# Kernel optimization log

Measured on AMD Instinct MI355X. Metric: run time of the kernel, lower is better.

The kernel has to match this reference:

```python
import jax, jax.numpy as jnp
import numpy as np

N_NODES, E, M_CELLS = 100000, 400000, 50000
D_IN, D_H, D_OUT = 384, 256, 256


def setup_inputs() -> dict:
    key = jax.random.key(0)
    ks = jax.random.split(key, 13)
    s = 0.02
    return {
        "chunk_features": jax.random.normal(ks[0], (N_NODES, D_IN), jnp.float32),
        "flat_nodes_t": jax.random.randint(ks[1], (E,), 0, N_NODES),
        "cell_asgn_t": jax.random.randint(ks[2], (E,), 0, M_CELLS),
        "M": M_CELLS,
        # phi: Linear(D_IN,D_H)+ReLU, Linear(D_H,D_H)+ReLU
        "W1": jax.random.normal(ks[3], (D_IN, D_H), jnp.float32) * s,
        "b1": jnp.zeros((D_H,), jnp.float32),
        "W2": jax.random.normal(ks[4], (D_H, D_H), jnp.float32) * s,
        "b2": jnp.zeros((D_H,), jnp.float32),
        # rho: Linear(D_H,D_H)+ReLU, Linear(D_H,D_H)+ReLU, Linear(D_H,D_OUT)
        "R1": jax.random.normal(ks[5], (D_H, D_H), jnp.float32) * s,
        "c1": jnp.zeros((D_H,), jnp.float32),
        "R2": jax.random.normal(ks[6], (D_H, D_H), jnp.float32) * s,
        "c2": jnp.zeros((D_H,), jnp.float32),
        "R3": jax.random.normal(ks[7], (D_H, D_OUT), jnp.float32) * s,
        "c3": jnp.zeros((D_OUT,), jnp.float32),
    }


def reference(chunk_features, flat_nodes_t, cell_asgn_t, M,
              W1, b1, W2, b2, R1, c1, R2, c2, R3, c3):
    # gather node features per cell-membership: [E, D_IN]
    x = chunk_features[flat_nodes_t]
    # phi MLP
    h = jax.nn.relu(x @ W1 + b1)
    h = jax.nn.relu(h @ W2 + b2)            # [E, D_H]
    # scatter-add per cell (torch scatter_add_ into zeros)
    cell_sums = jax.ops.segment_sum(h, cell_asgn_t, num_segments=M)  # [M, D_H]
    # rho MLP
    r = jax.nn.relu(cell_sums @ R1 + c1)
    r = jax.nn.relu(r @ R2 + c2)
    return r @ R3 + c3                      # [M, D_OUT]
```

## Files before the change

kernel.cpp:

```cpp
#include <hip/hip_runtime.h>

typedef unsigned short u16;
typedef __bf16 bf16x8 __attribute__((ext_vector_type(8)));
typedef float f32x4 __attribute__((ext_vector_type(4)));

__device__ __forceinline__ u16 f2bf(float f) {
  unsigned int u = __builtin_bit_cast(unsigned int, f);
  u += 0x7fffu + ((u >> 16) & 1u);
  return (u16)(u >> 16);
}
__device__ __forceinline__ float bf2f(u16 h) {
  unsigned int u = ((unsigned int)h) << 16;
  return __builtin_bit_cast(float, u);
}

__global__ __launch_bounds__(256) void k_prep(
    const float* __restrict__ W1, const float* __restrict__ W2,
    const float* __restrict__ R1, const float* __restrict__ R2, const float* __restrict__ R3,
    u16* __restrict__ W1s, u16* __restrict__ W2s,
    u16* __restrict__ R1s, u16* __restrict__ R2s, u16* __restrict__ R3s) {
  int t = blockIdx.x * 256 + threadIdx.x;
  const float* src; u16* dst; int lt;
  if (t < 12288) { src = W1; dst = W1s; lt = t; }
  else {
    int u = t - 12288;
    int m = u >> 13;
    lt = u & 8191;
    if (m == 0)      { src = W2; dst = W2s; }
    else if (m == 1) { src = R1; dst = R1s; }
    else if (m == 2) { src = R2; dst = R2s; }
    else if (m == 3) { src = R3; dst = R3s; }
    else return;
  }
  int lane = lt & 63;
  int nt = (lt >> 6) & 15;
  int ks = lt >> 10;
  int col = nt * 16 + (lane & 15);
  int kb = ks * 32 + (lane >> 4) * 8;
  union { u16 u[8]; uint4 v; } o;
#pragma unroll
  for (int j = 0; j < 8; ++j) o.u[j] = f2bf(src[(size_t)(kb + j) * 256 + col]);
  *(uint4*)(dst + (size_t)lt * 8) = o.v;
}

__global__ __launch_bounds__(256) void k_hist(const int* __restrict__ cells,
                                              int* __restrict__ counts, int E) {
  int e = blockIdx.x * 256 + threadIdx.x;
  if (e < E) atomicAdd(&counts[cells[e]], 1);
}

__global__ __launch_bounds__(256) void k_scan1(const int* __restrict__ counts,
                                               int* __restrict__ offs,
                                               int* __restrict__ bsum, int M) {
  __shared__ int ws[4];
  int tid = threadIdx.x, lane = tid & 63, wid = tid >> 6;
  int i = blockIdx.x * 256 + tid;
  int v = (i < M) ? counts[i] : 0;
  int x = v;
#pragma unroll
  for (int s = 1; s < 64; s <<= 1) { int y = __shfl_up(x, s); if (lane >= s) x += y; }
  if (lane == 63) ws[wid] = x;
  __syncthreads();
  int pre = 0;
#pragma unroll
  for (int w = 0; w < 4; ++w) if (w < wid) pre += ws[w];
  if (i < M) offs[i] = pre + x - v;
  if (tid == 255) bsum[blockIdx.x] = pre + x;
}

__global__ __launch_bounds__(256) void k_scan2(int* __restrict__ bsum, int nb) {
  __shared__ int ws[4];
  int tid = threadIdx.x, lane = tid & 63, wid = tid >> 6;
  int v = (tid < nb) ? bsum[tid] : 0;
  int x = v;
#pragma unroll
  for (int s = 1; s < 64; s <<= 1) { int y = __shfl_up(x, s); if (lane >= s) x += y; }
  if (lane == 63) ws[wid] = x;
  __syncthreads();
  int pre = 0;
#pragma unroll
  for (int w = 0; w < 4; ++w) if (w < wid) pre += ws[w];
  if (tid < nb) bsum[tid] = pre + x - v;
}

__global__ __launch_bounds__(256) void k_scan3(int* __restrict__ offs,
                                               const int* __restrict__ bsum,
                                               int* __restrict__ cursor, int M, int E) {
  int i = blockIdx.x * 256 + threadIdx.x;
  if (i < M) { int o = offs[i] + bsum[blockIdx.x]; offs[i] = o; cursor[i] = o; }
  if (i == M) offs[M] = E;
}

__global__ __launch_bounds__(256) void k_scatter(const int* __restrict__ cells,
                                                 const int* __restrict__ nodes,
                                                 int* __restrict__ cursor,
                                                 int* __restrict__ sorted, int E) {
  int e = blockIdx.x * 256 + threadIdx.x;
  if (e < E) {
    int c = cells[e];
    int p = atomicAdd(&cursor[c], 1);
    sorted[p] = nodes[e];
  }
}

__global__ __launch_bounds__(256) void k_phi(
    const float* __restrict__ X,
    const u16* __restrict__ W1s, const float* __restrict__ b1,
    const u16* __restrict__ W2s, const float* __restrict__ b2,
    u16* __restrict__ H, int N) {
  __shared__ __align__(16) u16 buf[64 * 256];
  const int tid = threadIdx.x, lane = tid & 63, wid = tid >> 6;
  const int g = lane >> 4, r16 = lane & 15;
  const int rbase = blockIdx.x * 64;
  const int swz = r16 << 3;

  const u16* w1p = W1s + (size_t)(wid * 4) * 512 + lane * 8;
  const u16* w2p = W2s + (size_t)(wid * 4) * 512 + lane * 8;

  {
    f32x4 xr[16];
#pragma unroll
    for (int it = 0; it < 16; ++it) {
      int u = it * 256 + tid;
      int row = u >> 6, c4 = u & 63;
      int crow = rbase + row; crow = crow < N ? crow : N - 1;
      xr[it] = *(const f32x4*)(X + (size_t)crow * 384 + c4 * 4);
    }
#pragma unroll
    for (int it = 0; it < 16; ++it) {
      int u = it * 256 + tid;
      int row = u >> 6, c4 = u & 63;
      uint2 pk;
      pk.x = (unsigned int)f2bf(xr[it][0]) | ((unsigned int)f2bf(xr[it][1]) << 16);
      pk.y = (unsigned int)f2bf(xr[it][2]) | ((unsigned int)f2bf(xr[it][3]) << 16);
      *(uint2*)(buf + row * 256 + ((c4 * 4) ^ ((row & 15) << 3))) = pk;
    }
  }
  __syncthreads();

  f32x4 acc[4][4];
#pragma unroll
  for (int m = 0; m < 4; ++m)
#pragma unroll
    for (int n = 0; n < 4; ++n) acc[m][n] = (f32x4){0.f, 0.f, 0.f, 0.f};

#pragma unroll 1
  for (int ks = 0; ks < 8; ++ks) {
    bf16x8 bfr[4];
#pragma unroll
    for (int n = 0; n < 4; ++n)
      bfr[n] = *(const bf16x8*)(w1p + (size_t)ks * 8192 + n * 512);
    const u16* bp = buf + ((ks * 32 + g * 8) ^ swz);
#pragma unroll
    for (int m = 0; m < 4; ++m) {
      bf16x8 af = *(const bf16x8*)(bp + (m * 16 + r16) * 256);
#pragma unroll
      for (int n = 0; n < 4; ++n)
        acc[m][n] = __builtin_amdgcn_mfma_f32_16x16x32_bf16(af, bfr[n], acc[m][n], 0, 0, 0);
    }
  }
  __syncthreads();

  {
    f32x4 xr[8];
#pragma unroll
    for (int it = 0; it < 8; ++it) {
      int u = it * 256 + tid;
      int row = u >> 5, c4 = u & 31;
      int crow = rbase + row; crow = crow < N ? crow : N - 1;
      xr[it] = *(const f32x4*)(X + (size_t)crow * 384 + 256 + c4 * 4);
    }
#pragma unroll
    for (int it = 0; it < 8; ++it) {
      int u = it * 256 + tid;
      int row = u >> 5, c4 = u & 31;
      uint2 pk;
      pk.x = (unsigned int)f2bf(xr[it][0]) | ((unsigned int)f2bf(xr[it][1]) << 16);
      pk.y = (unsigned int)f2bf(xr[it][2]) | ((unsigned int)f2bf(xr[it][3]) << 16);
      *(uint2*)(buf + row * 256 + ((c4 * 4) ^ ((row & 15) << 3))) = pk;
    }
  }
  __syncthreads();

#pragma unroll 1
  for (int ksl = 0; ksl < 4; ++ksl) {
    bf16x8 bfr[4];
#pragma unroll
    for (int n = 0; n < 4; ++n)
      bfr[n] = *(const bf16x8*)(w1p + (size_t)(8 + ksl) * 8192 + n * 512);
    const u16* bp = buf + ((ksl * 32 + g * 8) ^ swz);
#pragma unroll
    for (int m = 0; m < 4; ++m) {
      bf16x8 af = *(const bf16x8*)(bp + (m * 16 + r16) * 256);
#pragma unroll
      for (int n = 0; n < 4; ++n)
        acc[m][n] = __builtin_amdgcn_mfma_f32_16x16x32_bf16(af, bfr[n], acc[m][n], 0, 0, 0);
    }
  }
  __syncthreads();

  float bias1[4];
#pragma unroll
  for (int n = 0; n < 4; ++n) bias1[n] = b1[wid * 64 + n * 16 + r16];
#pragma unroll
  for (int m = 0; m < 4; ++m)
#pragma unroll
    for (int n = 0; n < 4; ++n)
#pragma unroll
      for (int rr = 0; rr < 4; ++rr) {
        int row = m * 16 + g * 4 + rr;
        int col = wid * 64 + n * 16 + r16;
        float v = fmaxf(acc[m][n][rr] + bias1[n], 0.f);
        buf[row * 256 + (col ^ ((row & 15) << 3))] = f2bf(v);
      }
  __syncthreads();

#pragma unroll
  for (int m = 0; m < 4; ++m)
#pragma unroll
    for (int n = 0; n < 4; ++n) acc[m][n] = (f32x4){0.f, 0.f, 0.f, 0.f};
#pragma unroll 1
  for (int ks = 0; ks < 8; ++ks) {
    bf16x8 bfr[4];
#pragma unroll
    for (int n = 0; n < 4; ++n)
      bfr[n] = *(const bf16x8*)(w2p + (size_t)ks * 8192 + n * 512);
    const u16* bp = buf + ((ks * 32 + g * 8) ^ swz);
#pragma unroll
    for (int m = 0; m < 4; ++m) {
      bf16x8 af = *(const bf16x8*)(bp + (m * 16 + r16) * 256);
#pragma unroll
      for (int n = 0; n < 4; ++n)
        acc[m][n] = __builtin_amdgcn_mfma_f32_16x16x32_bf16(af, bfr[n], acc[m][n], 0, 0, 0);
    }
  }
  __syncthreads();

  float bias2[4];
#pragma unroll
  for (int n = 0; n < 4; ++n) bias2[n] = b2[wid * 64 + n * 16 + r16];
#pragma unroll
  for (int m = 0; m < 4; ++m)
#pragma unroll
    for (int n = 0; n < 4; ++n)
#pragma unroll
      for (int rr = 0; rr < 4; ++rr) {
        int row = m * 16 + g * 4 + rr;
        int col = wid * 64 + n * 16 + r16;
        float v = fmaxf(acc[m][n][rr] + bias2[n], 0.f);
        buf[row * 256 + (col ^ ((row & 15) << 3))] = f2bf(v);
      }
  __syncthreads();

#pragma unroll 4
  for (int it = 0; it < 8; ++it) {
    int u = it * 256 + tid;
    int row = u >> 5, k8 = u & 31;
    uint4 d = *(const uint4*)(buf + row * 256 + ((k8 * 8) ^ ((row & 15) << 3)));
    int grow = rbase + row;
    if (grow < N) *(uint4*)(H + (size_t)grow * 256 + k8 * 8) = d;
  }
}

__global__ __launch_bounds__(256) void k_cellsum(
    const u16* __restrict__ H, const int* __restrict__ sorted,
    const int* __restrict__ offs, u16* __restrict__ CS, int M) {
  const int lane = threadIdx.x & 63, wid = threadIdx.x >> 6;
  int c = blockIdx.x * 4 + wid;
  if (c >= M) return;
  int s = offs[c], e = offs[c + 1];
  float a0 = 0.f, a1 = 0.f, a2 = 0.f, a3 = 0.f;
  for (int base = s; base < e; base += 64) {
    int cnt = e - base; if (cnt > 64) cnt = 64;
    int idx = sorted[base + (lane < cnt ? lane : 0)];
    int j = 0;
    for (; j + 8 <= cnt; j += 8) {
      ushort4 h[8];
#pragma unroll
      for (int q = 0; q < 8; ++q) {
        int nd = __shfl(idx, j + q);
        h[q] = *(const ushort4*)(H + (size_t)nd * 256 + lane * 4);
      }
#pragma unroll
      for (int q = 0; q < 8; ++q) {
        a0 += bf2f(h[q].x); a1 += bf2f(h[q].y);
        a2 += bf2f(h[q].z); a3 += bf2f(h[q].w);
      }
    }
    if (j + 4 <= cnt) {
      ushort4 h[4];
#pragma unroll
      for (int q = 0; q < 4; ++q) {
        int nd = __shfl(idx, j + q);
        h[q] = *(const ushort4*)(H + (size_t)nd * 256 + lane * 4);
      }
#pragma unroll
      for (int q = 0; q < 4; ++q) {
        a0 += bf2f(h[q].x); a1 += bf2f(h[q].y);
        a2 += bf2f(h[q].z); a3 += bf2f(h[q].w);
      }
      j += 4;
    }
    for (; j < cnt; ++j) {
      int nd = __shfl(idx, j);
      ushort4 h = *(const ushort4*)(H + (size_t)nd * 256 + lane * 4);
      a0 += bf2f(h.x); a1 += bf2f(h.y); a2 += bf2f(h.z); a3 += bf2f(h.w);
    }
  }
  ushort4 o;
  o.x = f2bf(a0); o.y = f2bf(a1); o.z = f2bf(a2); o.w = f2bf(a3);
  *(ushort4*)(CS + (size_t)c * 256 + lane * 4) = o;
}

__global__ __launch_bounds__(256) void k_rho(
    const u16* __restrict__ CS,
    const u16* __restrict__ R1s, const float* __restrict__ c1,
    const u16* __restrict__ R2s, const float* __restrict__ c2,
    const u16* __restrict__ R3s, const float* __restrict__ c3,
    float* __restrict__ OUT, int M) {
  __shared__ __align__(16) u16 buf[64 * 256];
  const int tid = threadIdx.x, lane = tid & 63, wid = tid >> 6;
  const int g = lane >> 4, r16 = lane & 15;
  const int rbase = blockIdx.x * 64;
  const int swz = r16 << 3;

  const u16* w1p = R1s + (size_t)(wid * 4) * 512 + lane * 8;
  const u16* w2p = R2s + (size_t)(wid * 4) * 512 + lane * 8;
  const u16* w3p = R3s + (size_t)(wid * 4) * 512 + lane * 8;

  {
    uint4 xr[8];
#pragma unroll
    for (int it = 0; it < 8; ++it) {
      int u = it * 256 + tid;
      int row = u >> 5, k8 = u & 31;
      int crow = rbase + row; crow = crow < M ? crow : M - 1;
      xr[it] = *(const uint4*)(CS + (size_t)crow * 256 + k8 * 8);
    }
#pragma unroll
    for (int it = 0; it < 8; ++it) {
      int u = it * 256 + tid;
      int row = u >> 5, k8 = u & 31;
      *(uint4*)(buf + row * 256 + ((k8 * 8) ^ ((row & 15) << 3))) = xr[it];
    }
  }
  __syncthreads();

  f32x4 acc[4][4];

#pragma unroll
  for (int m = 0; m < 4; ++m)
#pragma unroll
    for (int n = 0; n < 4; ++n) acc[m][n] = (f32x4){0.f, 0.f, 0.f, 0.f};
#pragma unroll 1
  for (int ks = 0; ks < 8; ++ks) {
    bf16x8 bfr[4];
#pragma unroll
    for (int n = 0; n < 4; ++n)
      bfr[n] = *(const bf16x8*)(w1p + (size_t)ks * 8192 + n * 512);
    const u16* bp = buf + ((ks * 32 + g * 8) ^ swz);
#pragma unroll
    for (int m = 0; m < 4; ++m) {
      bf16x8 af = *(const bf16x8*)(bp + (m * 16 + r16) * 256);
#pragma unroll
      for (int n = 0; n < 4; ++n)
        acc[m][n] = __builtin_amdgcn_mfma_f32_16x16x32_bf16(af, bfr[n], acc[m][n], 0, 0, 0);
    }
  }
  __syncthreads();

  float bias1[4];
#pragma unroll
  for (int n = 0; n < 4; ++n) bias1[n] = c1[wid * 64 + n * 16 + r16];
#pragma unroll
  for (int m = 0; m < 4; ++m)
#pragma unroll
    for (int n = 0; n < 4; ++n)
#pragma unroll
      for (int rr = 0; rr < 4; ++rr) {
        int row = m * 16 + g * 4 + rr;
        int col = wid * 64 + n * 16 + r16;
        float v = fmaxf(acc[m][n][rr] + bias1[n], 0.f);
        buf[row * 256 + (col ^ ((row & 15) << 3))] = f2bf(v);
      }
  __syncthreads();

#pragma unroll
  for (int m = 0; m < 4; ++m)
#pragma unroll
    for (int n = 0; n < 4; ++n) acc[m][n] = (f32x4){0.f, 0.f, 0.f, 0.f};
#pragma unroll 1
  for (int ks = 0; ks < 8; ++ks) {
    bf16x8 bfr[4];
#pragma unroll
    for (int n = 0; n < 4; ++n)
      bfr[n] = *(const bf16x8*)(w2p + (size_t)ks * 8192 + n * 512);
    const u16* bp = buf + ((ks * 32 + g * 8) ^ swz);
#pragma unroll
    for (int m = 0; m < 4; ++m) {
      bf16x8 af = *(const bf16x8*)(bp + (m * 16 + r16) * 256);
#pragma unroll
      for (int n = 0; n < 4; ++n)
        acc[m][n] = __builtin_amdgcn_mfma_f32_16x16x32_bf16(af, bfr[n], acc[m][n], 0, 0, 0);
    }
  }
  __syncthreads();

  float bias2[4];
#pragma unroll
  for (int n = 0; n < 4; ++n) bias2[n] = c2[wid * 64 + n * 16 + r16];
#pragma unroll
  for (int m = 0; m < 4; ++m)
#pragma unroll
    for (int n = 0; n < 4; ++n)
#pragma unroll
      for (int rr = 0; rr < 4; ++rr) {
        int row = m * 16 + g * 4 + rr;
        int col = wid * 64 + n * 16 + r16;
        float v = fmaxf(acc[m][n][rr] + bias2[n], 0.f);
        buf[row * 256 + (col ^ ((row & 15) << 3))] = f2bf(v);
      }
  __syncthreads();

#pragma unroll
  for (int m = 0; m < 4; ++m)
#pragma unroll
    for (int n = 0; n < 4; ++n) acc[m][n] = (f32x4){0.f, 0.f, 0.f, 0.f};
#pragma unroll 1
  for (int ks = 0; ks < 8; ++ks) {
    bf16x8 bfr[4];
#pragma unroll
    for (int n = 0; n < 4; ++n)
      bfr[n] = *(const bf16x8*)(w3p + (size_t)ks * 8192 + n * 512);
    const u16* bp = buf + ((ks * 32 + g * 8) ^ swz);
#pragma unroll
    for (int m = 0; m < 4; ++m) {
      bf16x8 af = *(const bf16x8*)(bp + (m * 16 + r16) * 256);
#pragma unroll
      for (int n = 0; n < 4; ++n)
        acc[m][n] = __builtin_amdgcn_mfma_f32_16x16x32_bf16(af, bfr[n], acc[m][n], 0, 0, 0);
    }
  }
#pragma unroll
  for (int n = 0; n < 4; ++n) {
    float bias = c3[wid * 64 + n * 16 + r16];
#pragma unroll
    for (int m = 0; m < 4; ++m)
#pragma unroll
      for (int rr = 0; rr < 4; ++rr) {
        int grow = rbase + m * 16 + g * 4 + rr;
        if (grow < M) OUT[(size_t)grow * 256 + wid * 64 + n * 16 + r16] = acc[m][n][rr] + bias;
      }
  }
}

extern "C" void kernel_launch(void* const* d_in, const int* in_sizes, int n_in,
                              void* d_out, int out_size, void* d_ws, size_t ws_size,
                              hipStream_t stream) {
  const float* X    = (const float*)d_in[0];
  const int* nodes  = (const int*)d_in[1];
  const int* cells  = (const int*)d_in[2];
  const float* W1   = (const float*)d_in[4];
  const float* b1   = (const float*)d_in[5];
  const float* W2   = (const float*)d_in[6];
  const float* b2   = (const float*)d_in[7];
  const float* R1   = (const float*)d_in[8];
  const float* c1   = (const float*)d_in[9];
  const float* R2   = (const float*)d_in[10];
  const float* c2   = (const float*)d_in[11];
  const float* R3   = (const float*)d_in[12];
  const float* c3   = (const float*)d_in[13];
  float* OUT = (float*)d_out;

  const int N = in_sizes[0] / 384;
  const int E = in_sizes[1];
  const int M = out_size / 256;

  char* ws = (char*)d_ws;
  size_t off = 0;
  auto alloc = [&](size_t b) { size_t o = off; off += (b + 255) & ~(size_t)255; return o; };
  u16* W1s    = (u16*)(ws + alloc((size_t)12 * 16 * 64 * 8 * 2));
  u16* W2s    = (u16*)(ws + alloc((size_t)8 * 16 * 64 * 8 * 2));
  u16* R1s    = (u16*)(ws + alloc((size_t)8 * 16 * 64 * 8 * 2));
  u16* R2s    = (u16*)(ws + alloc((size_t)8 * 16 * 64 * 8 * 2));
  u16* R3s    = (u16*)(ws + alloc((size_t)8 * 16 * 64 * 8 * 2));
  u16* H      = (u16*)(ws + alloc((size_t)N * 256 * 2));
  u16* CS     = (u16*)(ws + alloc((size_t)M * 256 * 2));
  int* counts = (int*)(ws + alloc((size_t)M * 4));
  int* offs   = (int*)(ws + alloc((size_t)(M + 1) * 4));
  int* cursor = (int*)(ws + alloc((size_t)M * 4));
  int* sorted = (int*)(ws + alloc((size_t)E * 4));
  int* bsum   = (int*)(ws + alloc((size_t)256 * 4));

  const int NB = (M + 255) / 256;

  hipMemsetAsync(counts, 0, (size_t)M * 4, stream);
  k_prep<<<176, 256, 0, stream>>>(W1, W2, R1, R2, R3, W1s, W2s, R1s, R2s, R3s);
  k_hist<<<(E + 255) / 256, 256, 0, stream>>>(cells, counts, E);
  k_scan1<<<NB, 256, 0, stream>>>(counts, offs, bsum, M);
  k_scan2<<<1, 256, 0, stream>>>(bsum, NB);
  k_scan3<<<(M + 256) / 256, 256, 0, stream>>>(offs, bsum, cursor, M, E);
  k_scatter<<<(E + 255) / 256, 256, 0, stream>>>(cells, nodes, cursor, sorted, E);
  k_phi<<<(N + 63) / 64, 256, 0, stream>>>(X, W1s, b1, W2s, b2, H, N);
  k_cellsum<<<(M + 3) / 4, 256, 0, stream>>>(H, sorted, offs, CS, M);
  k_rho<<<(M + 63) / 64, 256, 0, stream>>>(CS, R1s, c1, R2s, c2, R3s, c3, OUT, M);
}
```

Baseline: 222.0 us.

## Make phi and rho MLP kernels persistent with register-prefetched next tiles

Converts the phi and rho MLP kernels into persistent grid-stride loops over 32-row tiles, prefetching the next tile's inputs into registers while the current tile's GEMMs run, with separate LDS buffers for input and hidden activations. Biases are hoisted out of the loop, and the phi kernel stages the full 384-wide input at once instead of in two halves. The goal is to hide global-load latency behind MFMA work and cut per-block launch and prologue cost. In exchange each block uses smaller tiles with less weight reuse per tile, and the fixed grid sizes (1024 and 512 blocks) may not balance evenly across CUs.

```diff
diff --git a/kernel.cpp b/kernel.cpp
--- a/kernel.cpp
+++ b/kernel.cpp
@@ -108,157 +108,137 @@
     const u16* __restrict__ W1s, const float* __restrict__ b1,
     const u16* __restrict__ W2s, const float* __restrict__ b2,
     u16* __restrict__ H, int N) {
-  __shared__ __align__(16) u16 buf[64 * 256];
+  __shared__ __align__(16) u16 xbuf[32 * 384];
+  __shared__ __align__(16) u16 hbuf[32 * 256];
   const int tid = threadIdx.x, lane = tid & 63, wid = tid >> 6;
   const int g = lane >> 4, r16 = lane & 15;
-  const int rbase = blockIdx.x * 64;
   const int swz = r16 << 3;
+  const int T = (N + 31) >> 5;
+  const int step = gridDim.x;
 
   const u16* w1p = W1s + (size_t)(wid * 4) * 512 + lane * 8;
   const u16* w2p = W2s + (size_t)(wid * 4) * 512 + lane * 8;
 
-  {
-    f32x4 xr[16];
-#pragma unroll
-    for (int it = 0; it < 16; ++it) {
+  float bias1[4], bias2[4];
+#pragma unroll
+  for (int n = 0; n < 4; ++n) {
+    bias1[n] = b1[wid * 64 + n * 16 + r16];
+    bias2[n] = b2[wid * 64 + n * 16 + r16];
+  }
+
+  f32x4 xr[12];
+
+  auto issue = [&](int t) {
+#pragma unroll
+    for (int it = 0; it < 12; ++it) {
       int u = it * 256 + tid;
-      int row = u >> 6, c4 = u & 63;
-      int crow = rbase + row; crow = crow < N ? crow : N - 1;
+      int row = u / 96, c4 = u - row * 96;
+      int crow = t * 32 + row; crow = crow < N ? crow : N - 1;
       xr[it] = *(const f32x4*)(X + (size_t)crow * 384 + c4 * 4);
     }
-#pragma unroll
-    for (int it = 0; it < 16; ++it) {
+  };
+  auto stagewrite = [&]() {
+#pragma unroll
+    for (int it = 0; it < 12; ++it) {
       int u = it * 256 + tid;
-      int row = u >> 6, c4 = u & 63;
+      int row = u / 96, c4 = u - row * 96;
       uint2 pk;
       pk.x = (unsigned int)f2bf(xr[it][0]) | ((unsigned int)f2bf(xr[it][1]) << 16);
       pk.y = (unsigned int)f2bf(xr[it][2]) | ((unsigned int)f2bf(xr[it][3]) << 16);
-      *(uint2*)(buf + row * 256 + ((c4 * 4) ^ ((row & 15) << 3))) = pk;
-    }
-  }
+      *(uint2*)(xbuf + row * 384 + ((c4 * 4) ^ ((row & 15) << 3))) = pk;
+    }
+  };
+
+  const int t0 = blockIdx.x;
+  if (t0 >= T) return;
+
+  issue(t0);
+  stagewrite();
   __syncthreads();
-
-  f32x4 acc[4][4];
-#pragma unroll
-  for (int m = 0; m < 4; ++m)
-#pragma unroll
-    for (int n = 0; n < 4; ++n) acc[m][n] = (f32x4){0.f, 0.f, 0.f, 0.f};
-
-#pragma unroll 1
-  for (int ks = 0; ks < 8; ++ks) {
-    bf16x8 bfr[4];
-#pragma unroll
-    for (int n = 0; n < 4; ++n)
-      bfr[n] = *(const bf16x8*)(w1p + (size_t)ks * 8192 + n * 512);
-    const u16* bp = buf + ((ks * 32 + g * 8) ^ swz);
-#pragma unroll
-    for (int m = 0; m < 4; ++m) {
-      bf16x8 af = *(const bf16x8*)(bp + (m * 16 + r16) * 256);
-#pragma unroll
-      for (int n = 0; n < 4; ++n)
-        acc[m][n] = __builtin_amdgcn_mfma_f32_16x16x32_bf16(af, bfr[n], acc[m][n], 0, 0, 0);
-    }
-  }
-  __syncthreads();
-
-  {
-    f32x4 xr[8];
-#pragma unroll
-    for (int it = 0; it < 8; ++it) {
+  issue(t0 + step);
+
+  for (int t = t0; t < T; t += step) {
+    f32x4 acc[2][4];
+#pragma unroll
+    for (int m = 0; m < 2; ++m)
+#pragma unroll
+      for (int n = 0; n < 4; ++n) acc[m][n] = (f32x4){0.f, 0.f, 0.f, 0.f};
+#pragma unroll 4
+    for (int ks = 0; ks < 12; ++ks) {
+      bf16x8 bfr[4];
+#pragma unroll
+      for (int n = 0; n < 4; ++n)
+        bfr[n] = *(const bf16x8*)(w1p + (size_t)ks * 8192 + n * 512);
+      const u16* bp = xbuf + ((ks * 32 + g * 8) ^ swz);
+#pragma unroll
+      for (int m = 0; m < 2; ++m) {
+        bf16x8 af = *(const bf16x8*)(bp + (m * 16 + r16) * 384);
+#pragma unroll
+        for (int n = 0; n < 4; ++n)
+          acc[m][n] = __builtin_amdgcn_mfma_f32_16x16x32_bf16(af, bfr[n], acc[m][n], 0, 0, 0);
+      }
+    }
+    __syncthreads();
+
+    stagewrite();
+
+#pragma unroll
+    for (int m = 0; m < 2; ++m)
+#pragma unroll
+      for (int n = 0; n < 4; ++n)
+#pragma unroll
+        for (int rr = 0; rr < 4; ++rr) {
+          int row = m * 16 + g * 4 + rr;
+          int col = wid * 64 + n * 16 + r16;
+          float v = fmaxf(acc[m][n][rr] + bias1[n], 0.f);
+          hbuf[row * 256 + (col ^ ((row & 15) << 3))] = f2bf(v);
+        }
+    __syncthreads();
+
+    issue(t + 2 * step);
+
+#pragma unroll
+    for (int m = 0; m < 2; ++m)
+#pragma unroll
+      for (int n = 0; n < 4; ++n) acc[m][n] = (f32x4){0.f, 0.f, 0.f, 0.f};
+#pragma unroll 4
+    for (int ks = 0; ks < 8; ++ks) {
+      bf16x8 bfr[4];
+#pragma unroll
+      for (int n = 0; n < 4; ++n)
+        bfr[n] = *(const bf16x8*)(w2p + (size_t)ks * 8192 + n * 512);
+      const u16* bp = hbuf + ((ks * 32 + g * 8) ^ swz);
+#pragma unroll
+      for (int m = 0; m < 2; ++m) {
+        bf16x8 af = *(const bf16x8*)(bp + (m * 16 + r16) * 256);
+#pragma unroll
+        for (int n = 0; n < 4; ++n)
+          acc[m][n] = __builtin_amdgcn_mfma_f32_16x16x32_bf16(af, bfr[n], acc[m][n], 0, 0, 0);
+      }
+    }
+    __syncthreads();
+
+#pragma unroll
+    for (int m = 0; m < 2; ++m)
+#pragma unroll
+      for (int n = 0; n < 4; ++n)
+#pragma unroll
+        for (int rr = 0; rr < 4; ++rr) {
+          int row = m * 16 + g * 4 + rr;
+          int col = wid * 64 + n * 16 + r16;
+          float v = fmaxf(acc[m][n][rr] + bias2[n], 0.f);
+          hbuf[row * 256 + (col ^ ((row & 15) << 3))] = f2bf(v);
+        }
+    __syncthreads();
+
+#pragma unroll
+    for (int it = 0; it < 4; ++it) {
       int u = it * 256 + tid;
-      int row = u >> 5, c4 = u & 31;
-      int crow = rbase + row; crow = crow < N ? crow : N - 1;
-      xr[it] = *(const f32x4*)(X + (size_t)crow * 384 + 256 + c4 * 4);
-    }
-#pragma unroll
-    for (int it = 0; it < 8; ++it) {
-      int u = it * 256 + tid;
-      int row = u >> 5, c4 = u & 31;
-      uint2 pk;
-      pk.x = (unsigned int)f2bf(xr[it][0]) | ((unsigned int)f2bf(xr[it][1]) << 16);
-      pk.y = (unsigned int)f2bf(xr[it][2]) | ((unsigned int)f2bf(xr[it][3]) << 16);
-      *(uint2*)(buf + row * 256 + ((c4 * 4) ^ ((row & 15) << 3))) = pk;
-    }
-  }
-  __syncthreads();
-
-#pragma unroll 1
-  for (int ksl = 0; ksl < 4; ++ksl) {
-    bf16x8 bfr[4];
-#pragma unroll
-    for (int n = 0; n < 4; ++n)
-      bfr[n] = *(const bf16x8*)(w1p + (size_t)(8 + ksl) * 8192 + n * 512);
-    const u16* bp = buf + ((ksl * 32 + g * 8) ^ swz);
-#pragma unroll
-    for (int m = 0; m < 4; ++m) {
-      bf16x8 af = *(const bf16x8*)(bp + (m * 16 + r16) * 256);
-#pragma unroll
-      for (int n = 0; n < 4; ++n)
-        acc[m][n] = __builtin_amdgcn_mfma_f32_16x16x32_bf16(af, bfr[n], acc[m][n], 0, 0, 0);
-    }
-  }
-  __syncthreads();
-
-  float bias1[4];
-#pragma unroll
-  for (int n = 0; n < 4; ++n) bias1[n] = b1[wid * 64 + n * 16 + r16];
-#pragma unroll
-  for (int m = 0; m < 4; ++m)
-#pragma unroll
-    for (int n = 0; n < 4; ++n)
-#pragma unroll
-      for (int rr = 0; rr < 4; ++rr) {
-        int row = m * 16 + g * 4 + rr;
-        int col = wid * 64 + n * 16 + r16;
-        float v = fmaxf(acc[m][n][rr] + bias1[n], 0.f);
-        buf[row * 256 + (col ^ ((row & 15) << 3))] = f2bf(v);
-      }
-  __syncthreads();
-
-#pragma unroll
-  for (int m = 0; m < 4; ++m)
-#pragma unroll
-    for (int n = 0; n < 4; ++n) acc[m][n] = (f32x4){0.f, 0.f, 0.f, 0.f};
-#pragma unroll 1
-  for (int ks = 0; ks < 8; ++ks) {
-    bf16x8 bfr[4];
-#pragma unroll
-    for (int n = 0; n < 4; ++n)
-      bfr[n] = *(const bf16x8*)(w2p + (size_t)ks * 8192 + n * 512);
-    const u16* bp = buf + ((ks * 32 + g * 8) ^ swz);
-#pragma unroll
-    for (int m = 0; m < 4; ++m) {
-      bf16x8 af = *(const bf16x8*)(bp + (m * 16 + r16) * 256);
-#pragma unroll
-      for (int n = 0; n < 4; ++n)
-        acc[m][n] = __builtin_amdgcn_mfma_f32_16x16x32_bf16(af, bfr[n], acc[m][n], 0, 0, 0);
-    }
-  }
-  __syncthreads();
-
-  float bias2[4];
-#pragma unroll
-  for (int n = 0; n < 4; ++n) bias2[n] = b2[wid * 64 + n * 16 + r16];
-#pragma unroll
-  for (int m = 0; m < 4; ++m)
-#pragma unroll
-    for (int n = 0; n < 4; ++n)
-#pragma unroll
-      for (int rr = 0; rr < 4; ++rr) {
-        int row = m * 16 + g * 4 + rr;
-        int col = wid * 64 + n * 16 + r16;
-        float v = fmaxf(acc[m][n][rr] + bias2[n], 0.f);
-        buf[row * 256 + (col ^ ((row & 15) << 3))] = f2bf(v);
-      }
-  __syncthreads();
-
-#pragma unroll 4
-  for (int it = 0; it < 8; ++it) {
-    int u = it * 256 + tid;
-    int row = u >> 5, k8 = u & 31;
-    uint4 d = *(const uint4*)(buf + row * 256 + ((k8 * 8) ^ ((row & 15) << 3)));
-    int grow = rbase + row;
-    if (grow < N) *(uint4*)(H + (size_t)grow * 256 + k8 * 8) = d;
+      int row = u >> 5, k8 = u & 31;
+      uint4 d = *(const uint4*)(hbuf + row * 256 + ((k8 * 8) ^ ((row & 15) << 3)));
+      int grow = t * 32 + row;
+      if (grow < N) *(uint4*)(H + (size_t)grow * 256 + k8 * 8) = d;
+    }
   }
 }
 
@@ -318,139 +298,157 @@
     const u16* __restrict__ R2s, const float* __restrict__ c2,
     const u16* __restrict__ R3s, const float* __restrict__ c3,
     float* __restrict__ OUT, int M) {
-  __shared__ __align__(16) u16 buf[64 * 256];
+  __shared__ __align__(16) u16 xbuf[32 * 256];
+  __shared__ __align__(16) u16 hbuf[32 * 256];
   const int tid = threadIdx.x, lane = tid & 63, wid = tid >> 6;
   const int g = lane >> 4, r16 = lane & 15;
-  const int rbase = blockIdx.x * 64;
   const int swz = r16 << 3;
+  const int T = (M + 31) >> 5;
+  const int step = gridDim.x;
 
   const u16* w1p = R1s + (size_t)(wid * 4) * 512 + lane * 8;
   const u16* w2p = R2s + (size_t)(wid * 4) * 512 + lane * 8;
   const u16* w3p = R3s + (size_t)(wid * 4) * 512 + lane * 8;
 
-  {
-    uint4 xr[8];
-#pragma unroll
-    for (int it = 0; it < 8; ++it) {
+  float bias1[4], bias2[4], bias3[4];
+#pragma unroll
+  for (int n = 0; n < 4; ++n) {
+    bias1[n] = c1[wid * 64 + n * 16 + r16];
+    bias2[n] = c2[wid * 64 + n * 16 + r16];
+    bias3[n] = c3[wid * 64 + n * 16 + r16];
+  }
+
+  uint4 xr[4];
+  auto issue = [&](int t) {
+#pragma unroll
+    for (int it = 0; it < 4; ++it) {
       int u = it * 256 + tid;
       int row = u >> 5, k8 = u & 31;
-      int crow = rbase + row; crow = crow < M ? crow : M - 1;
+      int crow = t * 32 + row; crow = crow < M ? crow : M - 1;
       xr[it] = *(const uint4*)(CS + (size_t)crow * 256 + k8 * 8);
     }
-#pragma unroll
-    for (int it = 0; it < 8; ++it) {
+  };
+  auto stagewrite = [&]() {
+#pragma unroll
+    for (int it = 0; it < 4; ++it) {
       int u = it * 256 + tid;
       int row = u >> 5, k8 = u & 31;
-      *(uint4*)(buf + row * 256 + ((k8 * 8) ^ ((row & 15) << 3))) = xr[it];
-    }
-  }
+      *(uint4*)(xbuf + row * 256 + ((k8 * 8) ^ ((row & 15) << 3))) = xr[it];
+    }
+  };
+
+  const int t0 = blockIdx.x;
+  if (t0 >= T) return;
+  issue(t0);
+  stagewrite();
   __syncthreads();
-
-  f32x4 acc[4][4];
-
-#pragma unroll
-  for (int m = 0; m < 4; ++m)
-#pragma unroll
-    for (int n = 0; n < 4; ++n) acc[m][n] = (f32x4){0.f, 0.f, 0.f, 0.f};
-#pragma unroll 1
-  for (int ks = 0; ks < 8; ++ks) {
-    bf16x8 bfr[4];
-#pragma unroll
-    for (int n = 0; n < 4; ++n)
-      bfr[n] = *(const bf16x8*)(w1p + (size_t)ks * 8192 + n * 512);
-    const u16* bp = buf + ((ks * 32 + g * 8) ^ swz);
-#pragma unroll
-    for (int m = 0; m < 4; ++m) {
-      bf16x8 af = *(const bf16x8*)(bp + (m * 16 + r16) * 256);
-#pragma unroll
-      for (int n = 0; n < 4; ++n)
-        acc[m][n] = __builtin_amdgcn_mfma_f32_16x16x32_bf16(af, bfr[n], acc[m][n], 0, 0, 0);
-    }
-  }
-  __syncthreads();
-
-  float bias1[4];
-#pragma unroll
-  for (int n = 0; n < 4; ++n) bias1[n] = c1[wid * 64 + n * 16 + r16];
-#pragma unroll
-  for (int m = 0; m < 4; ++m)
-#pragma unroll
-    for (int n = 0; n < 4; ++n)
-#pragma unroll
-      for (int rr = 0; rr < 4; ++rr) {
-        int row = m * 16 + g * 4 + rr;
-        int col = wid * 64 + n * 16 + r16;
-        float v = fmaxf(acc[m][n][rr] + bias1[n], 0.f);
-        buf[row * 256 + (col ^ ((row & 15) << 3))] = f2bf(v);
-      }
-  __syncthreads();
-
-#pragma unroll
-  for (int m = 0; m < 4; ++m)
-#pragma unroll
-    for (int n = 0; n < 4; ++n) acc[m][n] = (f32x4){0.f, 0.f, 0.f, 0.f};
-#pragma unroll 1
-  for (int ks = 0; ks < 8; ++ks) {
-    bf16x8 bfr[4];
-#pragma unroll
-    for (int n = 0; n < 4; ++n)
-      bfr[n] = *(const bf16x8*)(w2p + (size_t)ks * 8192 + n * 512);
-    const u16* bp = buf + ((ks * 32 + g * 8) ^ swz);
-#pragma unroll
-    for (int m = 0; m < 4; ++m) {
-      bf16x8 af = *(const bf16x8*)(bp + (m * 16 + r16) * 256);
-#pragma unroll
-      for (int n = 0; n < 4; ++n)
-        acc[m][n] = __builtin_amdgcn_mfma_f32_16x16x32_bf16(af, bfr[n], acc[m][n], 0, 0, 0);
-    }
-  }
-  __syncthreads();
-
-  float bias2[4];
-#pragma unroll
-  for (int n = 0; n < 4; ++n) bias2[n] = c2[wid * 64 + n * 16 + r16];
-#pragma unroll
-  for (int m = 0; m < 4; ++m)
-#pragma unroll
-    for (int n = 0; n < 4; ++n)
-#pragma unroll
-      for (int rr = 0; rr < 4; ++rr) {
-        int row = m * 16 + g * 4 + rr;
-        int col = wid * 64 + n * 16 + r16;
-        float v = fmaxf(acc[m][n][rr] + bias2[n], 0.f);
-        buf[row * 256 + (col ^ ((row & 15) << 3))] = f2bf(v);
-      }
-  __syncthreads();
-
-#pragma unroll
-  for (int m = 0; m < 4; ++m)
-#pragma unroll
-    for (int n = 0; n < 4; ++n) acc[m][n] = (f32x4){0.f, 0.f, 0.f, 0.f};
-#pragma unroll 1
-  for (int ks = 0; ks < 8; ++ks) {
-    bf16x8 bfr[4];
-#pragma unroll
-    for (int n = 0; n < 4; ++n)
-      bfr[n] = *(const bf16x8*)(w3p + (size_t)ks * 8192 + n * 512);
-    const u16* bp = buf + ((ks * 32 + g * 8) ^ swz);
-#pragma unroll
-    for (int m = 0; m < 4; ++m) {
-      bf16x8 af = *(const bf16x8*)(bp + (m * 16 + r16) * 256);
-#pragma unroll
-      for (int n = 0; n < 4; ++n)
-        acc[m][n] = __builtin_amdgcn_mfma_f32_16x16x32_bf16(af, bfr[n], acc[m][n], 0, 0, 0);
-    }
-  }
-#pragma unroll
-  for (int n = 0; n < 4; ++n) {
-    float bias = c3[wid * 64 + n * 16 + r16];
-#pragma unroll
-    for (int m = 0; m < 4; ++m)
-#pragma unroll
-      for (int rr = 0; rr < 4; ++rr) {
-        int grow = rbase + m * 16 + g * 4 + rr;
-        if (grow < M) OUT[(size_t)grow * 256 + wid * 64 + n * 16 + r16] = acc[m][n][rr] + bias;
-      }
+  issue(t0 + step);
+
+  for (int t = t0; t < T; t += step) {
+    f32x4 acc[2][4];
+
+#pragma unroll
+    for (int m = 0; m < 2; ++m)
+#pragma unroll
+      for (int n = 0; n < 4; ++n) acc[m][n] = (f32x4){0.f, 0.f, 0.f, 0.f};
+#pragma unroll 4
+    for (int ks = 0; ks < 8; ++ks) {
+      bf16x8 bfr[4];
+#pragma unroll
+      for (int n = 0; n < 4; ++n)
+        bfr[n] = *(const bf16x8*)(w1p + (size_t)ks * 8192 + n * 512);
+      const u16* bp = xbuf + ((ks * 32 + g * 8) ^ swz);
+#pragma unroll
+      for (int m = 0; m < 2; ++m) {
+        bf16x8 af = *(const bf16x8*)(bp + (m * 16 + r16) * 256);
+#pragma unroll
+        for (int n = 0; n < 4; ++n)
+          acc[m][n] = __builtin_amdgcn_mfma_f32_16x16x32_bf16(af, bfr[n], acc[m][n], 0, 0, 0);
+      }
+    }
+    __syncthreads();
+
+    stagewrite();
+
+#pragma unroll
+    for (int m = 0; m < 2; ++m)
+#pragma unroll
+      for (int n = 0; n < 4; ++n)
+#pragma unroll
+        for (int rr = 0; rr < 4; ++rr) {
+          int row = m * 16 + g * 4 + rr;
+          int col = wid * 64 + n * 16 + r16;
+          float v = fmaxf(acc[m][n][rr] + bias1[n], 0.f);
+          hbuf[row * 256 + (col ^ ((row & 15) << 3))] = f2bf(v);
+        }
+    __syncthreads();
+
+    issue(t + 2 * step);
+
+#pragma unroll
+    for (int m = 0; m < 2; ++m)
+#pragma unroll
+      for (int n = 0; n < 4; ++n) acc[m][n] = (f32x4){0.f, 0.f, 0.f, 0.f};
+#pragma unroll 4
+    for (int ks = 0; ks < 8; ++ks) {
+      bf16x8 bfr[4];
+#pragma unroll
+      for (int n = 0; n < 4; ++n)
+        bfr[n] = *(const bf16x8*)(w2p + (size_t)ks * 8192 + n * 512);
+      const u16* bp = hbuf + ((ks * 32 + g * 8) ^ swz);
+#pragma unroll
+      for (int m = 0; m < 2; ++m) {
+        bf16x8 af = *(const bf16x8*)(bp + (m * 16 + r16) * 256);
+#pragma unroll
+        for (int n = 0; n < 4; ++n)
+          acc[m][n] = __builtin_amdgcn_mfma_f32_16x16x32_bf16(af, bfr[n], acc[m][n], 0, 0, 0);
+      }
+    }
+    __syncthreads();
+
+#pragma unroll
+    for (int m = 0; m < 2; ++m)
+#pragma unroll
+      for (int n = 0; n < 4; ++n)
+#pragma unroll
+        for (int rr = 0; rr < 4; ++rr) {
+          int row = m * 16 + g * 4 + rr;
+          int col = wid * 64 + n * 16 + r16;
+          float v = fmaxf(acc[m][n][rr] + bias2[n], 0.f);
+          hbuf[row * 256 + (col ^ ((row & 15) << 3))] = f2bf(v);
+        }
+    __syncthreads();
+
+#pragma unroll
+    for (int m = 0; m < 2; ++m)
+#pragma unroll
+      for (int n = 0; n < 4; ++n) acc[m][n] = (f32x4){0.f, 0.f, 0.f, 0.f};
+#pragma unroll 4
+    for (int ks = 0; ks < 8; ++ks) {
+      bf16x8 bfr[4];
+#pragma unroll
+      for (int n = 0; n < 4; ++n)
+        bfr[n] = *(const bf16x8*)(w3p + (size_t)ks * 8192 + n * 512);
+      const u16* bp = hbuf + ((ks * 32 + g * 8) ^ swz);
+#pragma unroll
+      for (int m = 0; m < 2; ++m) {
+        bf16x8 af = *(const bf16x8*)(bp + (m * 16 + r16) * 256);
+#pragma unroll
+        for (int n = 0; n < 4; ++n)
+          acc[m][n] = __builtin_amdgcn_mfma_f32_16x16x32_bf16(af, bfr[n], acc[m][n], 0, 0, 0);
+      }
+    }
+#pragma unroll
+    for (int n = 0; n < 4; ++n) {
+#pragma unroll
+      for (int m = 0; m < 2; ++m)
+#pragma unroll
+        for (int rr = 0; rr < 4; ++rr) {
+          int grow = t * 32 + m * 16 + g * 4 + rr;
+          if (grow < M)
+            OUT[(size_t)grow * 256 + wid * 64 + n * 16 + r16] = acc[m][n][rr] + bias3[n];
+        }
+    }
   }
 }
 
@@ -501,7 +499,7 @@
   k_scan2<<<1, 256, 0, stream>>>(bsum, NB);
   k_scan3<<<(M + 256) / 256, 256, 0, stream>>>(offs, bsum, cursor, M, E);
   k_scatter<<<(E + 255) / 256, 256, 0, stream>>>(cells, nodes, cursor, sorted, E);
-  k_phi<<<(N + 63) / 64, 256, 0, stream>>>(X, W1s, b1, W2s, b2, H, N);
+  k_phi<<<1024, 256, 0, stream>>>(X, W1s, b1, W2s, b2, H, N);
   k_cellsum<<<(M + 3) / 4, 256, 0, stream>>>(H, sorted, offs, CS, M);
-  k_rho<<<(M + 63) / 64, 256, 0, stream>>>(CS, R1s, c1, R2s, c2, R3s, c3, OUT, M);
-}
+  k_rho<<<512, 256, 0, stream>>>(CS, R1s, c1, R2s, c2, R3s, c3, OUT, M);
+}
```

After: 219.0 us. About the same (-1.3%).

## Use 1024-thread blocks with 128-row tiles in phi and rho MLP kernels

Applied to the files above, without the earlier changes.

Both fused MLP kernels now process 128 rows per block with 16 waves instead of 64 rows with 4 waves. Each wave owns one 16-column slice across all 128 rows, so it loads one weight fragment per k-step and reuses it across 8 row tiles. The aim is to halve weight traffic per row and amortise the activation staging over more rows. The cost is a larger LDS buffer (64KB), fewer accumulators and fewer weight fragments per wave, and possibly lower occupancy with 1024-thread blocks.

```diff
diff --git a/kernel.cpp b/kernel.cpp
--- a/kernel.cpp
+++ b/kernel.cpp
@@ -103,32 +103,35 @@
   }
 }
 
-__global__ __launch_bounds__(256) void k_phi(
+__global__ __launch_bounds__(1024) void k_phi_big(
     const float* __restrict__ X,
     const u16* __restrict__ W1s, const float* __restrict__ b1,
     const u16* __restrict__ W2s, const float* __restrict__ b2,
     u16* __restrict__ H, int N) {
-  __shared__ __align__(16) u16 buf[64 * 256];
+  __shared__ __align__(16) u16 buf[128 * 256];
   const int tid = threadIdx.x, lane = tid & 63, wid = tid >> 6;
   const int g = lane >> 4, r16 = lane & 15;
-  const int rbase = blockIdx.x * 64;
   const int swz = r16 << 3;
-
-  const u16* w1p = W1s + (size_t)(wid * 4) * 512 + lane * 8;
-  const u16* w2p = W2s + (size_t)(wid * 4) * 512 + lane * 8;
+  const int rbase = blockIdx.x * 128;
+
+  const u16* w1p = W1s + (size_t)wid * 512 + lane * 8;
+  const u16* w2p = W2s + (size_t)wid * 512 + lane * 8;
+
+  const float bias1 = b1[wid * 16 + r16];
+  const float bias2 = b2[wid * 16 + r16];
 
   {
-    f32x4 xr[16];
-#pragma unroll
-    for (int it = 0; it < 16; ++it) {
-      int u = it * 256 + tid;
+    f32x4 xr[8];
+#pragma unroll
+    for (int it = 0; it < 8; ++it) {
+      int u = it * 1024 + tid;
       int row = u >> 6, c4 = u & 63;
       int crow = rbase + row; crow = crow < N ? crow : N - 1;
       xr[it] = *(const f32x4*)(X + (size_t)crow * 384 + c4 * 4);
     }
 #pragma unroll
-    for (int it = 0; it < 16; ++it) {
-      int u = it * 256 + tid;
+    for (int it = 0; it < 8; ++it) {
+      int u = it * 1024 + tid;
       int row = u >> 6, c4 = u & 63;
       uint2 pk;
       pk.x = (unsigned int)f2bf(xr[it][0]) | ((unsigned int)f2bf(xr[it][1]) << 16);
@@ -138,41 +141,34 @@
   }
   __syncthreads();
 
-  f32x4 acc[4][4];
-#pragma unroll
-  for (int m = 0; m < 4; ++m)
-#pragma unroll
-    for (int n = 0; n < 4; ++n) acc[m][n] = (f32x4){0.f, 0.f, 0.f, 0.f};
-
-#pragma unroll 1
+  f32x4 acc[8];
+#pragma unroll
+  for (int m = 0; m < 8; ++m) acc[m] = (f32x4){0.f, 0.f, 0.f, 0.f};
+
+#pragma unroll 2
   for (int ks = 0; ks < 8; ++ks) {
-    bf16x8 bfr[4];
-#pragma unroll
-    for (int n = 0; n < 4; ++n)
-      bfr[n] = *(const bf16x8*)(w1p + (size_t)ks * 8192 + n * 512);
+    bf16x8 bfr = *(const bf16x8*)(w1p + (size_t)ks * 8192);
     const u16* bp = buf + ((ks * 32 + g * 8) ^ swz);
 #pragma unroll
-    for (int m = 0; m < 4; ++m) {
-      bf16x8 af = *(const bf16x8*)(bp + (m * 16 + r16) * 256);
-#pragma unroll
-      for (int n = 0; n < 4; ++n)
-        acc[m][n] = __builtin_amdgcn_mfma_f32_16x16x32_bf16(af, bfr[n], acc[m][n], 0, 0, 0);
+    for (int m = 0; m < 8; ++m) {
+      bf16x8 af = *(const bf16x8*)(bp + (m * 16 + r16) * 256);
+      acc[m] = __builtin_amdgcn_mfma_f32_16x16x32_bf16(af, bfr, acc[m], 0, 0, 0);
     }
   }
   __syncthreads();
 
   {
-    f32x4 xr[8];
-#pragma unroll
-    for (int it = 0; it < 8; ++it) {
-      int u = it * 256 + tid;
+    f32x4 xr[4];
+#pragma unroll
+    for (int it = 0; it < 4; ++it) {
+      int u = it * 1024 + tid;
       int row = u >> 5, c4 = u & 31;
       int crow = rbase + row; crow = crow < N ? crow : N - 1;
       xr[it] = *(const f32x4*)(X + (size_t)crow * 384 + 256 + c4 * 4);
     }
 #pragma unroll
-    for (int it = 0; it < 8; ++it) {
-      int u = it * 256 + tid;
+    for (int it = 0; it < 4; ++it) {
+      int u = it * 1024 + tid;
       int row = u >> 5, c4 = u & 31;
       uint2 pk;
       pk.x = (unsigned int)f2bf(xr[it][0]) | ((unsigned int)f2bf(xr[it][1]) << 16);
@@ -182,79 +178,57 @@
   }
   __syncthreads();
 
-#pragma unroll 1
+#pragma unroll
   for (int ksl = 0; ksl < 4; ++ksl) {
-    bf16x8 bfr[4];
-#pragma unroll
-    for (int n = 0; n < 4; ++n)
-      bfr[n] = *(const bf16x8*)(w1p + (size_t)(8 + ksl) * 8192 + n * 512);
+    bf16x8 bfr = *(const bf16x8*)(w1p + (size_t)(8 + ksl) * 8192);
     const u16* bp = buf + ((ksl * 32 + g * 8) ^ swz);
 #pragma unroll
-    for (int m = 0; m < 4; ++m) {
-      bf16x8 af = *(const bf16x8*)(bp + (m * 16 + r16) * 256);
-#pragma unroll
-      for (int n = 0; n < 4; ++n)
-        acc[m][n] = __builtin_amdgcn_mfma_f32_16x16x32_bf16(af, bfr[n], acc[m][n], 0, 0, 0);
-    }
-  }
-  __syncthreads();
-
-  float bias1[4];
-#pragma unroll
-  for (int n = 0; n < 4; ++n) bias1[n] = b1[wid * 64 + n * 16 + r16];
-#pragma unroll
-  for (int m = 0; m < 4; ++m)
-#pragma unroll
-    for (int n = 0; n < 4; ++n)
-#pragma unroll
-      for (int rr = 0; rr < 4; ++rr) {
-        int row = m * 16 + g * 4 + rr;
-        int col = wid * 64 + n * 16 + r16;
-        float v = fmaxf(acc[m][n][rr] + bias1[n], 0.f);
-        buf[row * 256 + (col ^ ((row & 15) << 3))] = f2bf(v);
-      }
-  __syncthreads();
-
-#pragma unroll
-  for (int m = 0; m < 4; ++m)
-#pragma unroll
-    for (int n = 0; n < 4; ++n) acc[m][n] = (f32x4){0.f, 0.f, 0.f, 0.f};
-#pragma unroll 1
+    for (int m = 0; m < 8; ++m) {
+      bf16x8 af = *(const bf16x8*)(bp + (m * 16 + r16) * 256);
+      acc[m] = __builtin_amdgcn_mfma_f32_16x16x32_bf16(af, bfr, acc[m], 0, 0, 0);
+    }
+  }
+  __syncthreads();
+
+#pragma unroll
+  for (int m = 0; m < 8; ++m)
+#pragma unroll
+    for (int rr = 0; rr < 4; ++rr) {
+      int row = m * 16 + g * 4 + rr;
+      int col = wid * 16 + r16;
+      float v = fmaxf(acc[m][rr] + bias1, 0.f);
+      buf[row * 256 + (col ^ ((row & 15) << 3))] = f2bf(v);
+    }
+  __syncthreads();
+
+#pragma unroll
+  for (int m = 0; m < 8; ++m) acc[m] = (f32x4){0.f, 0.f, 0.f, 0.f};
+#pragma unroll 2
   for (int ks = 0; ks < 8; ++ks) {
-    bf16x8 bfr[4];
-#pragma unroll
-    for (int n = 0; n < 4; ++n)
-      bfr[n] = *(const bf16x8*)(w2p + (size_t)ks * 8192 + n * 512);
+    bf16x8 bfr = *(const bf16x8*)(w2p + (size_t)ks * 8192);
     const u16* bp = buf + ((ks * 32 + g * 8) ^ swz);
 #pragma unroll
-    for (int m = 0; m < 4; ++m) {
-      bf16x8 af = *(const bf16x8*)(bp + (m * 16 + r16) * 256);
-#pragma unroll
-      for (int n = 0; n < 4; ++n)
-        acc[m][n] = __builtin_amdgcn_mfma_f32_16x16x32_bf16(af, bfr[n], acc[m][n], 0, 0, 0);
-    }
-  }
-  __syncthreads();
-
-  float bias2[4];
-#pragma unroll
-  for (int n = 0; n < 4; ++n) bias2[n] = b2[wid * 64 + n * 16 + r16];
-#pragma unroll
-  for (int m = 0; m < 4; ++m)
-#pragma unroll
-    for (int n = 0; n < 4; ++n)
-#pragma unroll
-      for (int rr = 0; rr < 4; ++rr) {
-        int row = m * 16 + g * 4 + rr;
-        int col = wid * 64 + n * 16 + r16;
-        float v = fmaxf(acc[m][n][rr] + bias2[n], 0.f);
-        buf[row * 256 + (col ^ ((row & 15) << 3))] = f2bf(v);
-      }
-  __syncthreads();
-
-#pragma unroll 4
-  for (int it = 0; it < 8; ++it) {
-    int u = it * 256 + tid;
+    for (int m = 0; m < 8; ++m) {
+      bf16x8 af = *(const bf16x8*)(bp + (m * 16 + r16) * 256);
+      acc[m] = __builtin_amdgcn_mfma_f32_16x16x32_bf16(af, bfr, acc[m], 0, 0, 0);
+    }
+  }
+  __syncthreads();
+
+#pragma unroll
+  for (int m = 0; m < 8; ++m)
+#pragma unroll
+    for (int rr = 0; rr < 4; ++rr) {
+      int row = m * 16 + g * 4 + rr;
+      int col = wid * 16 + r16;
+      float v = fmaxf(acc[m][rr] + bias2, 0.f);
+      buf[row * 256 + (col ^ ((row & 15) << 3))] = f2bf(v);
+    }
+  __syncthreads();
+
+#pragma unroll
+  for (int it = 0; it < 4; ++it) {
+    int u = it * 1024 + tid;
     int row = u >> 5, k8 = u & 31;
     uint4 d = *(const uint4*)(buf + row * 256 + ((k8 * 8) ^ ((row & 15) << 3)));
     int grow = rbase + row;
@@ -312,146 +286,116 @@
   *(ushort4*)(CS + (size_t)c * 256 + lane * 4) = o;
 }
 
-__global__ __launch_bounds__(256) void k_rho(
+__global__ __launch_bounds__(1024) void k_rho_big(
     const u16* __restrict__ CS,
     const u16* __restrict__ R1s, const float* __restrict__ c1,
     const u16* __restrict__ R2s, const float* __restrict__ c2,
     const u16* __restrict__ R3s, const float* __restrict__ c3,
     float* __restrict__ OUT, int M) {
-  __shared__ __align__(16) u16 buf[64 * 256];
+  __shared__ __align__(16) u16 buf[128 * 256];
   const int tid = threadIdx.x, lane = tid & 63, wid = tid >> 6;
   const int g = lane >> 4, r16 = lane & 15;
-  const int rbase = blockIdx.x * 64;
   const int swz = r16 << 3;
-
-  const u16* w1p = R1s + (size_t)(wid * 4) * 512 + lane * 8;
-  const u16* w2p = R2s + (size_t)(wid * 4) * 512 + lane * 8;
-  const u16* w3p = R3s + (size_t)(wid * 4) * 512 + lane * 8;
+  const int rbase = blockIdx.x * 128;
+
+  const u16* w1p = R1s + (size_t)wid * 512 + lane * 8;
+  const u16* w2p = R2s + (size_t)wid * 512 + lane * 8;
+  const u16* w3p = R3s + (size_t)wid * 512 + lane * 8;
+
+  const float bias1 = c1[wid * 16 + r16];
+  const float bias2 = c2[wid * 16 + r16];
+  const float bias3 = c3[wid * 16 + r16];
 
   {
-    uint4 xr[8];
-#pragma unroll
-    for (int it = 0; it < 8; ++it) {
-      int u = it * 256 + tid;
+    uint4 xr[4];
+#pragma unroll
+    for (int it = 0; it < 4; ++it) {
+      int u = it * 1024 + tid;
       int row = u >> 5, k8 = u & 31;
       int crow = rbase + row; crow = crow < M ? crow : M - 1;
       xr[it] = *(const uint4*)(CS + (size_t)crow * 256 + k8 * 8);
     }
 #pragma unroll
-    for (int it = 0; it < 8; ++it) {
-      int u = it * 256 + tid;
+    for (int it = 0; it < 4; ++it) {
+      int u = it * 1024 + tid;
       int row = u >> 5, k8 = u & 31;
       *(uint4*)(buf + row * 256 + ((k8 * 8) ^ ((row & 15) << 3))) = xr[it];
     }
   }
   __syncthreads();
 
-  f32x4 acc[4][4];
-
-#pragma unroll
-  for (int m = 0; m < 4; ++m)
-#pragma unroll
-    for (int n = 0; n < 4; ++n) acc[m][n] = (f32x4){0.f, 0.f, 0.f, 0.f};
-#pragma unroll 1
+  f32x4 acc[8];
+
+#pragma unroll
+  for (int m = 0; m < 8; ++m) acc[m] = (f32x4){0.f, 0.f, 0.f, 0.f};
+#pragma unroll 2
   for (int ks = 0; ks < 8; ++ks) {
-    bf16x8 bfr[4];
-#pragma unroll
-    for (int n = 0; n < 4; ++n)
-      bfr[n] = *(const bf16x8*)(w1p + (size_t)ks * 8192 + n * 512);
+    bf16x8 bfr = *(const bf16x8*)(w1p + (size_t)ks * 8192);
     const u16* bp = buf + ((ks * 32 + g * 8) ^ swz);
 #pragma unroll
-    for (int m = 0; m < 4; ++m) {
-      bf16x8 af = *(const bf16x8*)(bp + (m * 16 + r16) * 256);
-#pragma unroll
-      for (int n = 0; n < 4; ++n)
-        acc[m][n] = __builtin_amdgcn_mfma_f32_16x16x32_bf16(af, bfr[n], acc[m][n], 0, 0, 0);
-    }
-  }
-  __syncthreads();
-
-  float bias1[4];
-#pragma unroll
-  for (int n = 0; n < 4; ++n) bias1[n] = c1[wid * 64 + n * 16 + r16];
-#pragma unroll
-  for (int m = 0; m < 4; ++m)
-#pragma unroll
-    for (int n = 0; n < 4; ++n)
-#pragma unroll
-      for (int rr = 0; rr < 4; ++rr) {
-        int row = m * 16 + g * 4 + rr;
-        int col = wid * 64 + n * 16 + r16;
-        float v = fmaxf(acc[m][n][rr] + bias1[n], 0.f);
-        buf[row * 256 + (col ^ ((row & 15) << 3))] = f2bf(v);
-      }
-  __syncthreads();
-
-#pragma unroll
-  for (int m = 0; m < 4; ++m)
-#pragma unroll
-    for (int n = 0; n < 4; ++n) acc[m][n] = (f32x4){0.f, 0.f, 0.f, 0.f};
-#pragma unroll 1
+    for (int m = 0; m < 8; ++m) {
+      bf16x8 af = *(const bf16x8*)(bp + (m * 16 + r16) * 256);
+      acc[m] = __builtin_amdgcn_mfma_f32_16x16x32_bf16(af, bfr, acc[m], 0, 0, 0);
+    }
+  }
+  __syncthreads();
+
+#pragma unroll
+  for (int m = 0; m < 8; ++m)
+#pragma unroll
+    for (int rr = 0; rr < 4; ++rr) {
+      int row = m * 16 + g * 4 + rr;
+      int col = wid * 16 + r16;
+      float v = fmaxf(acc[m][rr] + bias1, 0.f);
+      buf[row * 256 + (col ^ ((row & 15) << 3))] = f2bf(v);
+    }
+  __syncthreads();
+
+#pragma unroll
+  for (int m = 0; m < 8; ++m) acc[m] = (f32x4){0.f, 0.f, 0.f, 0.f};
+#pragma unroll 2
   for (int ks = 0; ks < 8; ++ks) {
-    bf16x8 bfr[4];
-#pragma unroll
-    for (int n = 0; n < 4; ++n)
-      bfr[n] = *(const bf16x8*)(w2p + (size_t)ks * 8192 + n * 512);
+    bf16x8 bfr = *(const bf16x8*)(w2p + (size_t)ks * 8192);
     const u16* bp = buf + ((ks * 32 + g * 8) ^ swz);
 #pragma unroll
-    for (int m = 0; m < 4; ++m) {
-      bf16x8 af = *(const bf16x8*)(bp + (m * 16 + r16) * 256);
-#pragma unroll
-      for (int n = 0; n < 4; ++n)
-        acc[m][n] = __builtin_amdgcn_mfma_f32_16x16x32_bf16(af, bfr[n], acc[m][n], 0, 0, 0);
-    }
-  }
-  __syncthreads();
-
-  float bias2[4];
-#pragma unroll
-  for (int n = 0; n < 4; ++n) bias2[n] = c2[wid * 64 + n * 16 + r16];
-#pragma unroll
-  for (int m = 0; m < 4; ++m)
-#pragma unroll
-    for (int n = 0; n < 4; ++n)
-#pragma unroll
-      for (int rr = 0; rr < 4; ++rr) {
-        int row = m * 16 + g * 4 + rr;
-        int col = wid * 64 + n * 16 + r16;
-        float v = fmaxf(acc[m][n][rr] + bias2[n], 0.f);
-        buf[row * 256 + (col ^ ((row & 15) << 3))] = f2bf(v);
-      }
-  __syncthreads();
-
-#pragma unroll
-  for (int m = 0; m < 4; ++m)
-#pragma unroll
-    for (int n = 0; n < 4; ++n) acc[m][n] = (f32x4){0.f, 0.f, 0.f, 0.f};
-#pragma unroll 1
+    for (int m = 0; m < 8; ++m) {
+      bf16x8 af = *(const bf16x8*)(bp + (m * 16 + r16) * 256);
+      acc[m] = __builtin_amdgcn_mfma_f32_16x16x32_bf16(af, bfr, acc[m], 0, 0, 0);
+    }
+  }
+  __syncthreads();
+
+#pragma unroll
+  for (int m = 0; m < 8; ++m)
+#pragma unroll
+    for (int rr = 0; rr < 4; ++rr) {
+      int row = m * 16 + g * 4 + rr;
+      int col = wid * 16 + r16;
+      float v = fmaxf(acc[m][rr] + bias2, 0.f);
+      buf[row * 256 + (col ^ ((row & 15) << 3))] = f2bf(v);
+    }
+  __syncthreads();
+
+#pragma unroll
+  for (int m = 0; m < 8; ++m) acc[m] = (f32x4){0.f, 0.f, 0.f, 0.f};
+#pragma unroll 2
   for (int ks = 0; ks < 8; ++ks) {
-    bf16x8 bfr[4];
-#pragma unroll
-    for (int n = 0; n < 4; ++n)
-      bfr[n] = *(const bf16x8*)(w3p + (size_t)ks * 8192 + n * 512);
+    bf16x8 bfr = *(const bf16x8*)(w3p + (size_t)ks * 8192);
     const u16* bp = buf + ((ks * 32 + g * 8) ^ swz);
 #pragma unroll
-    for (int m = 0; m < 4; ++m) {
-      bf16x8 af = *(const bf16x8*)(bp + (m * 16 + r16) * 256);
-#pragma unroll
-      for (int n = 0; n < 4; ++n)
-        acc[m][n] = __builtin_amdgcn_mfma_f32_16x16x32_bf16(af, bfr[n], acc[m][n], 0, 0, 0);
-    }
-  }
-#pragma unroll
-  for (int n = 0; n < 4; ++n) {
-    float bias = c3[wid * 64 + n * 16 + r16];
-#pragma unroll
-    for (int m = 0; m < 4; ++m)
-#pragma unroll
-      for (int rr = 0; rr < 4; ++rr) {
-        int grow = rbase + m * 16 + g * 4 + rr;
-        if (grow < M) OUT[(size_t)grow * 256 + wid * 64 + n * 16 + r16] = acc[m][n][rr] + bias;
-      }
-  }
+    for (int m = 0; m < 8; ++m) {
+      bf16x8 af = *(const bf16x8*)(bp + (m * 16 + r16) * 256);
+      acc[m] = __builtin_amdgcn_mfma_f32_16x16x32_bf16(af, bfr, acc[m], 0, 0, 0);
+    }
+  }
+#pragma unroll
+  for (int m = 0; m < 8; ++m)
+#pragma unroll
+    for (int rr = 0; rr < 4; ++rr) {
+      int grow = rbase + m * 16 + g * 4 + rr;
+      if (grow < M)
+        OUT[(size_t)grow * 256 + wid * 16 + r16] = acc[m][rr] + bias3;
+    }
 }
 
 extern "C" void kernel_launch(void* const* d_in, const int* in_sizes, int n_in,
@@ -501,7 +445,7 @@
   k_scan2<<<1, 256, 0, stream>>>(bsum, NB);
   k_scan3<<<(M + 256) / 256, 256, 0, stream>>>(offs, bsum, cursor, M, E);
   k_scatter<<<(E + 255) / 256, 256, 0, stream>>>(cells, nodes, cursor, sorted, E);
-  k_phi<<<(N + 63) / 64, 256, 0, stream>>>(X, W1s, b1, W2s, b2, H, N);
+  k_phi_big<<<(N + 127) / 128, 1024, 0, stream>>>(X, W1s, b1, W2s, b2, H, N);
   k_cellsum<<<(M + 3) / 4, 256, 0, stream>>>(H, sorted, offs, CS, M);
-  k_rho<<<(M + 63) / 64, 256, 0, stream>>>(CS, R1s, c1, R2s, c2, R3s, c3, OUT, M);
-}
+  k_rho_big<<<(M + 127) / 128, 1024, 0, stream>>>(CS, R1s, c1, R2s, c2, R3s, c3, OUT, M);
+}
```

New measurement: 202.6 us. 1.1x faster.
